# Kernel optimization log

Hardware: AMD Instinct MI355X
Metric: run time of the kernel (lower is better)

Reference implementation:

```python
import jax, jax.numpy as jnp
import numpy as np

STRIDES = (4, 8, 16, 32, 64)
FEAT = ((128, 128), (64, 64), (32, 32), (16, 16), (8, 8))
RATIOS = np.array([0.5, 1.0, 2.0], dtype=np.float64)
SCALE = 8.0
PRE_NMS = 2000
MAX_PER_IMG = 1000
NMS_THR = 0.7
MAX_SHAPE = (512, 512)
MAX_RATIO = float(abs(np.log(16.0 / 1000.0)))  # mmdet wh_ratio_clip default


def grid_anchors(H, W, stride):
    # mmdet AnchorGenerator: base_size = stride, center_offset = 0
    h_ratios = np.sqrt(RATIOS)
    w_ratios = 1.0 / h_ratios
    ws = stride * w_ratios * SCALE
    hs = stride * h_ratios * SCALE
    base = np.stack([-0.5 * ws, -0.5 * hs, 0.5 * ws, 0.5 * hs], axis=1)  # (A,4)
    sx = np.arange(W) * stride
    sy = np.arange(H) * stride
    yy, xx = np.meshgrid(sy, sx, indexing='ij')  # x varies fastest (mmdet order)
    shifts = np.stack([xx, yy, xx, yy], axis=-1).reshape(-1, 4)  # (H*W,4)
    return jnp.asarray((shifts[:, None, :] + base[None, :, :]).reshape(-1, 4), jnp.float32)


def level_candidates(cls, reg, anchors):
    # cls: (A,H,W), reg: (4A,H,W) -> location-major, anchor-minor flatten
    scores = jax.nn.sigmoid(jnp.transpose(cls, (1, 2, 0)).reshape(-1))
    deltas = jnp.transpose(reg, (1, 2, 0)).reshape(-1, 4)
    k = min(PRE_NMS, scores.shape[0])
    scores, idx = jax.lax.top_k(scores, k)
    return scores, deltas[idx], anchors[idx]


def decode(anchors, deltas):
    # DeltaXYWHBBoxCoder.decode with means=0, stds=1, max_shape=(512,512)
    px = (anchors[..., 0] + anchors[..., 2]) * 0.5
    py = (anchors[..., 1] + anchors[..., 3]) * 0.5
    pw = anchors[..., 2] - anchors[..., 0]
    ph = anchors[..., 3] - anchors[..., 1]
    dx, dy = deltas[..., 0], deltas[..., 1]
    dw = jnp.clip(deltas[..., 2], -MAX_RATIO, MAX_RATIO)
    dh = jnp.clip(deltas[..., 3], -MAX_RATIO, MAX_RATIO)
    gw = pw * jnp.exp(dw)
    gh = ph * jnp.exp(dh)
    gx = px + pw * dx
    gy = py + ph * dy
    x1 = jnp.clip(gx - gw * 0.5, 0.0, MAX_SHAPE[1])
    y1 = jnp.clip(gy - gh * 0.5, 0.0, MAX_SHAPE[0])
    x2 = jnp.clip(gx + gw * 0.5, 0.0, MAX_SHAPE[1])
    y2 = jnp.clip(gy + gh * 0.5, 0.0, MAX_SHAPE[0])
    return jnp.stack([x1, y1, x2, y2], axis=-1)


def nms_image(boxes, scores, levels):
    # boxes (M,4), scores (M,), levels (M,) int32. Fixed-shape greedy batched NMS;
    # invalid (zero-size, cf. filter_boxes with min_area=0) boxes get score -1 and are never kept.
    M = scores.shape[0]
    valid = ((boxes[:, 2] - boxes[:, 0]) > 0) & ((boxes[:, 3] - boxes[:, 1]) > 0)
    s = jnp.where(valid, scores, -1.0)
    order = jnp.argsort(-s)
    boxes_s = boxes[order]
    s = s[order]
    valid = valid[order]
    lev = levels[order]
    # batched_nms trick: offset each level so boxes of different levels never overlap
    off = lev.astype(boxes.dtype)[:, None] * (MAX_SHAPE[0] + 1.0)
    b = boxes_s + off
    x1, y1, x2, y2 = b[:, 0], b[:, 1], b[:, 2], b[:, 3]
    area = (x2 - x1) * (y2 - y1)
    iw = jnp.maximum(jnp.minimum(x2[:, None], x2[None, :]) - jnp.maximum(x1[:, None], x1[None, :]), 0.0)
    ih = jnp.maximum(jnp.minimum(y2[:, None], y2[None, :]) - jnp.maximum(y1[:, None], y1[None, :]), 0.0)
    inter = iw * ih
    union = area[:, None] + area[None, :] - inter
    iou = jnp.where(union > 0.0, inter / jnp.where(union > 0.0, union, 1.0), 0.0)  # (M,M)
    ar = jnp.arange(M)

    def body(i, keep):
        sup = keep[i] & (iou[i] > NMS_THR) & (ar > i)
        return keep & ~sup

    keep = jax.lax.fori_loop(0, M, body, valid)
    rank = jnp.cumsum(keep) - 1
    sel = keep & (rank < MAX_PER_IMG)
    dst = jnp.where(sel, rank, MAX_PER_IMG)  # overflow slot
    rows = jnp.concatenate([boxes_s, s[:, None]], axis=-1)
    rows = jnp.where(sel[:, None], rows, 0.0)
    out = jnp.zeros((MAX_PER_IMG + 1, 5), boxes.dtype).at[dst].set(rows)
    return out[:MAX_PER_IMG]


def setup_inputs() -> dict:
    key = jax.random.key(0)
    ks = jax.random.split(key, 10)
    d = {}
    for i, (h, w) in enumerate(FEAT):
        d[f'cls{i}'] = jax.random.normal(ks[i], (4, 3, h, w), dtype=jnp.float32)
        d[f'reg{i}'] = jax.random.normal(ks[5 + i], (4, 12, h, w), dtype=jnp.float32)
    return d


def reference(cls0, cls1, cls2, cls3, cls4, reg0, reg1, reg2, reg3, reg4):
    cls_list = [cls0, cls1, cls2, cls3, cls4]
    reg_list = [reg0, reg1, reg2, reg3, reg4]
    anchors = [grid_anchors(h, w, s) for (h, w), s in zip(FEAT, STRIDES)]
    sc, dl, an, lv = [], [], [], []
    for lvl in range(5):
        s, d, a = jax.vmap(level_candidates, in_axes=(0, 0, None))(cls_list[lvl], reg_list[lvl], anchors[lvl])
        sc.append(s); dl.append(d); an.append(a)
        lv.append(jnp.full(s.shape, lvl, jnp.int32))
    scores = jnp.concatenate(sc, axis=1)   # (N, M)
    deltas = jnp.concatenate(dl, axis=1)   # (N, M, 4)
    ancs = jnp.concatenate(an, axis=1)     # (N, M, 4)
    levels = jnp.concatenate(lv, axis=1)   # (N, M)
    boxes = decode(ancs, deltas)           # (N, M, 4)
    return jax.vmap(nms_image)(boxes, scores, levels)  # (N, 1000, 5)
```

## Files before the change

kernel.cpp:

```cpp
#include <hip/hip_runtime.h>
#include <cstdint>
#include <cstddef>

__constant__ int LV_N[5]    = {49152, 12288, 3072, 768, 192};
__constant__ int LV_K[5]    = {2000, 2000, 2000, 768, 192};
__constant__ int LV_OFF[5]  = {0, 2000, 4000, 6000, 6768};
__constant__ int LV_UOFF[5] = {0, 49152, 61440, 64512, 65280};
__constant__ int LV_W[5]    = {128, 64, 32, 16, 8};
__constant__ int LV_S[5]    = {4, 8, 16, 32, 64};
__constant__ int LV_LOGHW[5]= {14, 12, 10, 8, 6};
__constant__ int WPL[5]     = {32, 32, 32, 12, 3};
__constant__ int MOFF[5]    = {0, 70144, 140288, 210432, 221952};
__constant__ int MB_BASE[6] = {0, 256, 512, 768, 804, 807};
__constant__ int MB_CT[5]   = {8, 8, 8, 3, 1};
__constant__ int SGB6[6]    = {0, 12, 15, 16, 17, 18};

#define M_TOT 6960
#define U_PER_IMG 65472
#define MAX_OUT 1000
#define MWORDS_PER_IMG 223104
#define CAP 4096

struct Ptrs { const float* cls[5]; const float* reg[5]; };

#define MTH 0.7000000178813934326171875

__device__ __forceinline__ float xla_expf(float x) {
  const float exp_hi = 88.3762626647950f;
  const float exp_lo = -88.3762626647949f;
  const float log2ef = 1.44269504088896341f;
  const float c1 = 0.693359375f;
  const float c2 = -2.12194440e-4f;
  const float p0 = 1.9875691500e-4f;
  const float p1 = 1.3981999507e-3f;
  const float p2 = 8.3334519073e-3f;
  const float p3 = 4.1665795894e-2f;
  const float p4 = 1.6666665459e-1f;
  const float p5 = 5.0000001201e-1f;
  float xx = fminf(fmaxf(x, exp_lo), exp_hi);
  float fx = floorf(__fmaf_rn(xx, log2ef, 0.5f));
  float r = __fmaf_rn(fx, -c1, xx);
  r = __fmaf_rn(fx, -c2, r);
  float z = __fmul_rn(r, r);
  float y = __fmaf_rn(p0, r, p1);
  y = __fmaf_rn(y, r, p2);
  y = __fmaf_rn(y, r, p3);
  y = __fmaf_rn(y, r, p4);
  y = __fmaf_rn(y, r, p5);
  y = __fmaf_rn(y, z, r);
  y = __fadd_rn(y, 1.0f);
  int n = (int)fx;
  float two_n = __uint_as_float((unsigned)(n + 127) << 23);
  return __fmul_rn(y, two_n);
}

__device__ __forceinline__ float ref_sigmoid(float x) {
  return __fdiv_rn(1.0f, __fadd_rn(1.0f, xla_expf(-x)));
}

__global__ __launch_bounds__(256) void k_zero(uint4* ptr, int n4) {
  int i = (int)blockIdx.x * 256 + (int)threadIdx.x;
  if (i < n4) ptr[i] = make_uint4(0u, 0u, 0u, 0u);
}

__global__ __launch_bounds__(1024) void k_sig(Ptrs p, unsigned* u_arr,
                                              unsigned* ghist) {
  const int img = blockIdx.y;
  const int bx = blockIdx.x;
  int lvl = 0;
  while (bx >= SGB6[lvl + 1]) ++lvl;
  const int N = LV_N[lvl];
  const int e0 = (bx - SGB6[lvl]) * 4096;
  const int e1 = (e0 + 4096 < N) ? e0 + 4096 : N;
  const int tid = (int)threadIdx.x;
  __shared__ unsigned h[4096];
  for (int e = tid; e < 4096; e += 1024) h[e] = 0;
  __syncthreads();
  const float* cls = p.cls[lvl] + (size_t)img * N;
  unsigned* u = u_arr + img * U_PER_IMG + LV_UOFF[lvl];
  for (int e = e0 + tid; e < e1; e += 1024) {
    float logit = cls[e];
    unsigned ub = __float_as_uint(ref_sigmoid(logit));
    u[e] = ub;
    atomicAdd(&h[(ub >> 18) & 4095u], 1u);
  }
  __syncthreads();
  unsigned* gh = ghist + (size_t)(img * 5 + lvl) * 4096;
  for (int e = tid; e < 4096; e += 1024)
    if (h[e]) atomicAdd(&gh[e], h[e]);
}

__global__ __launch_bounds__(1024) void k_thresh(const unsigned* u_arr,
    const unsigned* ghist, unsigned long long* T64_arr) {
  const int blk = blockIdx.x;
  const int img = blk / 5, lvl = blk % 5;
  const int N = LV_N[lvl], K = LV_K[lvl], LOGHW = LV_LOGHW[lvl];
  const int HW = 1 << LOGHW;
  const int tid = (int)threadIdx.x;
  const int lane = tid & 63, w = tid >> 6;
  if (N <= K) { if (tid == 0) T64_arr[blk] = 0ULL; return; }
  __shared__ unsigned h[4096];
  __shared__ unsigned wsum[16], wsuf[16];
  __shared__ unsigned sh_D, sh_sD, sh_sD1;
  const unsigned* u = u_arr + img * U_PER_IMG + LV_UOFF[lvl];

  unsigned long long prefix = 0;
  unsigned want = (unsigned)K, above = 0;
  const int shifts[6] = {50, 38, 26, 14, 2, 0};
  for (int rd = 0; rd < 6; ++rd) {
    const int shift = shifts[rd];
    if (rd == 5) {
      for (int e = tid; e < 4; e += 1024) h[e] = 0;
      __syncthreads();
      for (int q = tid; q < N; q += 1024) {
        unsigned a = (unsigned)q >> LOGHW, pix = (unsigned)q & (unsigned)(HW - 1);
        unsigned ecl = pix * 3u + a;
        unsigned long long key =
            ((unsigned long long)u[q] << 32) | (unsigned)(~ecl);
        if ((key >> 2) == prefix) atomicAdd(&h[(unsigned)key & 3u], 1u);
      }
      __syncthreads();
      if (tid == 0) {
        unsigned cum = 0; int D = 0;
        for (int v = 3; v >= 0; --v) {
          if (cum + h[v] >= want) { D = v; break; }
          cum += h[v];
        }
        T64_arr[blk] = (prefix << 2) | (unsigned)D;
      }
      return;
    }
    if (rd == 0) {
      for (int e = tid; e < 4096; e += 1024)
        h[e] = ghist[(size_t)blk * 4096 + e];
    } else {
      for (int e = tid; e < 4096; e += 1024) h[e] = 0;
      __syncthreads();
      for (int q = tid; q < N; q += 1024) {
        unsigned a = (unsigned)q >> LOGHW, pix = (unsigned)q & (unsigned)(HW - 1);
        unsigned ecl = pix * 3u + a;
        unsigned long long key =
            ((unsigned long long)u[q] << 32) | (unsigned)(~ecl);
        if ((key >> (shift + 12)) == prefix)
          atomicAdd(&h[(unsigned)(key >> shift) & 4095u], 1u);
      }
    }
    __syncthreads();
    unsigned h0 = h[4 * tid + 0], h1 = h[4 * tid + 1];
    unsigned h2 = h[4 * tid + 2], h3 = h[4 * tid + 3];
    unsigned s = h0 + h1 + h2 + h3;
    unsigned suf = s;
    #pragma unroll
    for (int off = 1; off < 64; off <<= 1) {
      unsigned t2 = __shfl_down(suf, off);
      if (lane + off < 64) suf += t2;
    }
    if (lane == 0) wsum[w] = suf;
    __syncthreads();
    if (tid < 16) {
      unsigned v = wsum[tid];
      #pragma unroll
      for (int off = 1; off < 16; off <<= 1) {
        unsigned t2 = __shfl_down(v, off);
        if (tid + off < 16) v += t2;
      }
      wsuf[tid] = v;
    }
    __syncthreads();
    unsigned Sth = ((w + 1 < 16) ? wsuf[w + 1] : 0u) + (suf - s);
    unsigned f3 = Sth + h3;
    unsigned f2 = f3 + h2;
    unsigned f1 = f2 + h1;
    unsigned f0 = f1 + h0;
    if (f0 >= want && f1 < want) { sh_D = 4u * tid + 0; sh_sD = f0; sh_sD1 = f1; }
    if (f1 >= want && f2 < want) { sh_D = 4u * tid + 1; sh_sD = f1; sh_sD1 = f2; }
    if (f2 >= want && f3 < want) { sh_D = 4u * tid + 2; sh_sD = f2; sh_sD1 = f3; }
    if (f3 >= want && Sth < want) { sh_D = 4u * tid + 3; sh_sD = f3; sh_sD1 = Sth; }
    __syncthreads();
    unsigned D = sh_D, sD = sh_sD, sD1 = sh_sD1;
    unsigned long long npref = (prefix << 12) | (unsigned long long)D;
    if (above + sD <= (unsigned)CAP) {
      if (tid == 0) T64_arr[blk] = npref << shift;
      return;
    }
    above += sD1; want -= sD1; prefix = npref;
    __syncthreads();
  }
}

__global__ __launch_bounds__(1024) void k_collect(const unsigned* u_arr,
    const unsigned long long* T64_arr, unsigned long long* gtk, unsigned* gcnt) {
  const int img = blockIdx.y;
  const int bx = blockIdx.x;
  int lvl = 0;
  while (bx >= SGB6[lvl + 1]) ++lvl;
  const int N = LV_N[lvl], LOGHW = LV_LOGHW[lvl];
  const int HW = 1 << LOGHW;
  const int e0 = (bx - SGB6[lvl]) * 4096;
  const int tid = (int)threadIdx.x;
  const int lane = tid & 63;
  const int w = tid >> 6;
  const unsigned long long T = T64_arr[img * 5 + lvl];
  const unsigned* u = u_arr + img * U_PER_IMG + LV_UOFF[lvl];

  __shared__ unsigned wcnt[64];

  unsigned long long key0 = 0, key1 = 0, key2 = 0, key3 = 0;
  unsigned long long bm0, bm1, bm2, bm3;
  #define MKKEY(KV, Q)                                                      \
    {                                                                       \
      unsigned a_ = (unsigned)(Q) >> LOGHW;                                 \
      unsigned pix_ = (unsigned)(Q) & (unsigned)(HW - 1);                   \
      unsigned ecl_ = pix_ * 3u + a_;                                       \
      KV = ((unsigned long long)u[Q] << 32) | (unsigned)(~ecl_);            \
    }
  {
    int q = e0 + 0 * 1024 + tid;
    bool pr = false;
    if (q < N) { MKKEY(key0, q) pr = key0 >= T; }
    bm0 = __ballot(pr);
    if (lane == 0) wcnt[w * 4 + 0] = (unsigned)__popcll(bm0);
  }
  {
    int q = e0 + 1 * 1024 + tid;
    bool pr = false;
    if (q < N) { MKKEY(key1, q) pr = key1 >= T; }
    bm1 = __ballot(pr);
    if (lane == 0) wcnt[w * 4 + 1] = (unsigned)__popcll(bm1);
  }
  {
    int q = e0 + 2 * 1024 + tid;
    bool pr = false;
    if (q < N) { MKKEY(key2, q) pr = key2 >= T; }
    bm2 = __ballot(pr);
    if (lane == 0) wcnt[w * 4 + 2] = (unsigned)__popcll(bm2);
  }
  {
    int q = e0 + 3 * 1024 + tid;
    bool pr = false;
    if (q < N) { MKKEY(key3, q) pr = key3 >= T; }
    bm3 = __ballot(pr);
    if (lane == 0) wcnt[w * 4 + 3] = (unsigned)__popcll(bm3);
  }
  #undef MKKEY
  __syncthreads();
  if (tid < 64) {
    unsigned c = wcnt[tid];
    unsigned pre = c;
    #pragma unroll
    for (int off = 1; off < 64; off <<= 1) {
      unsigned t = __shfl_up(pre, off);
      if (tid >= off) pre += t;
    }
    unsigned total = __shfl(pre, 63);
    unsigned base = 0;
    if (tid == 63 && total) base = atomicAdd(gcnt + (img * 5 + lvl), total);
    base = __shfl(base, 63);
    wcnt[tid] = base + pre - c;
  }
  __syncthreads();
  unsigned long long* dst = gtk + (size_t)(img * 5 + lvl) * CAP;
  const unsigned long long below = (1ULL << lane) - 1ULL;
  if ((bm0 >> lane) & 1ULL) {
    unsigned slot = wcnt[w * 4 + 0] + (unsigned)__popcll(bm0 & below);
    if (slot < (unsigned)CAP) dst[slot] = key0;
  }
  if ((bm1 >> lane) & 1ULL) {
    unsigned slot = wcnt[w * 4 + 1] + (unsigned)__popcll(bm1 & below);
    if (slot < (unsigned)CAP) dst[slot] = key1;
  }
  if ((bm2 >> lane) & 1ULL) {
    unsigned slot = wcnt[w * 4 + 2] + (unsigned)__popcll(bm2 & below);
    if (slot < (unsigned)CAP) dst[slot] = key2;
  }
  if ((bm3 >> lane) & 1ULL) {
    unsigned slot = wcnt[w * 4 + 3] + (unsigned)__popcll(bm3 & below);
    if (slot < (unsigned)CAP) dst[slot] = key3;
  }
}

__global__ __launch_bounds__(256) void k_rank(Ptrs p,
    const unsigned long long* gtk, const unsigned* gcnt,
    float* cand_box, float* cand_s, unsigned long long* vflags) {
  const int il = (int)blockIdx.y;
  const int img = il / 5, lvl = il % 5;
  const int N = LV_N[lvl], K = LV_K[lvl], W = LV_W[lvl], S = LV_S[lvl];
  const int HW = N / 3;
  const float* reg = p.reg[lvl] + (size_t)img * 12 * HW;
  const int tid = (int)threadIdx.x;
  unsigned cnt = gcnt[il];
  if (cnt > (unsigned)CAP) cnt = CAP;
  if ((unsigned)blockIdx.x * 256u >= cnt) return;
  const unsigned cnt32 = (cnt + 31u) & ~31u;
  __shared__ ulonglong2 keys2[CAP / 2];
  unsigned long long* keys = (unsigned long long*)keys2;
  const unsigned long long* src = gtk + (size_t)il * CAP;
  for (int e = tid; e < (int)cnt32; e += 256)
    keys[e] = (e < (int)cnt) ? src[e] : 0ULL;
  __syncthreads();
  const int s = (int)blockIdx.x * 256 + tid;
  if (s >= (int)cnt) return;
  const unsigned long long mykey = keys[s];
  unsigned r0 = 0, r1 = 0, r2 = 0, r3 = 0;
  const unsigned half = cnt32 >> 1;
  for (unsigned j = 0; j < half; j += 16) {
    #pragma unroll
    for (int q = 0; q < 16; q += 4) {
      ulonglong2 a = keys2[j + q + 0];
      ulonglong2 b = keys2[j + q + 1];
      ulonglong2 cc = keys2[j + q + 2];
      ulonglong2 d = keys2[j + q + 3];
      r0 += (a.x > mykey ? 1u : 0u) + (a.y > mykey ? 1u : 0u);
      r1 += (b.x > mykey ? 1u : 0u) + (b.y > mykey ? 1u : 0u);
      r2 += (cc.x > mykey ? 1u : 0u) + (cc.y > mykey ? 1u : 0u);
      r3 += (d.x > mykey ? 1u : 0u) + (d.y > mykey ? 1u : 0u);
    }
  }
  unsigned rank = r0 + r1 + r2 + r3;
  if (rank >= (unsigned)K) return;

  unsigned ubits = (unsigned)(mykey >> 32);
  unsigned idx = ~((unsigned)mykey);
  int a = (int)(idx % 3u); int pix = (int)(idx / 3u);
  int xq = pix % W, yq = pix / W;
  float dx = reg[(a * 4 + 0) * HW + pix];
  float dy = reg[(a * 4 + 1) * HW + pix];
  float dw = reg[(a * 4 + 2) * HW + pix];
  float dh = reg[(a * 4 + 3) * HW + pix];
  double rr = (a == 0) ? 0.5 : (a == 1 ? 1.0 : 2.0);
  double hr = sqrt(rr), wr = 1.0 / hr;
  double st = (double)S;
  double wsd = st * wr * 8.0, hsd = st * hr * 8.0;
  double sxd = (double)(xq * S), syd = (double)(yq * S);
  float a0 = (float)(sxd - 0.5 * wsd), a1 = (float)(syd - 0.5 * hsd);
  float a2 = (float)(sxd + 0.5 * wsd), a3 = (float)(syd + 0.5 * hsd);
  float px = __fmul_rn(__fadd_rn(a0, a2), 0.5f);
  float py = __fmul_rn(__fadd_rn(a1, a3), 0.5f);
  float pw = __fsub_rn(a2, a0), ph = __fsub_rn(a3, a1);
  const float MRf = 4.135166556742356f;
  float dwc = fminf(fmaxf(dw, -MRf), MRf);
  float dhc = fminf(fmaxf(dh, -MRf), MRf);
  float gw = __fmul_rn(pw, xla_expf(dwc));
  float gh = __fmul_rn(ph, xla_expf(dhc));
  float gx = __fmaf_rn(pw, dx, px);
  float gy = __fmaf_rn(ph, dy, py);
  float x1 = fminf(fmaxf(__fmaf_rn(gw, -0.5f, gx), 0.0f), 512.0f);
  float y1 = fminf(fmaxf(__fmaf_rn(gh, -0.5f, gy), 0.0f), 512.0f);
  float x2 = fminf(fmaxf(__fmaf_rn(gw,  0.5f, gx), 0.0f), 512.0f);
  float y2 = fminf(fmaxf(__fmaf_rn(gh,  0.5f, gy), 0.0f), 512.0f);
  bool valid = (__fsub_rn(x2, x1) > 0.0f) && (__fsub_rn(y2, y1) > 0.0f);
  int pos = img * M_TOT + LV_OFF[lvl] + (int)rank;
  cand_box[(size_t)pos * 4 + 0] = x1;
  cand_box[(size_t)pos * 4 + 1] = y1;
  cand_box[(size_t)pos * 4 + 2] = x2;
  cand_box[(size_t)pos * 4 + 3] = y2;
  float score = __uint_as_float(ubits);
  cand_s[pos] = valid ? score : -1.0f;
  if (valid)
    atomicOr(&vflags[(size_t)il * 32 + (rank >> 6)], 1ULL << (rank & 63));
}

__global__ __launch_bounds__(256) void k_part(const float* cand_box,
    const float* cand_s, const unsigned long long* vflags,
    float* n_x1, float* n_y1, float* n_x2, float* n_y2, float* n_ar,
    float* n_sc, unsigned* n_pos, unsigned* V_arr) {
  const int il = (int)blockIdx.x;
  const int img = il / 5, lvl = il % 5;
  const int K = LV_K[lvl];
  const int tid = (int)threadIdx.x;
  __shared__ unsigned long long sflag[32];
  __shared__ unsigned wpre[33];
  if (tid < 32) sflag[tid] = vflags[(size_t)il * 32 + tid];
  __syncthreads();
  if (tid < 32) {
    unsigned c = (unsigned)__popcll(sflag[tid]);
    #pragma unroll
    for (int off = 1; off < 32; off <<= 1) {
      unsigned t = __shfl_up(c, off);
      if (tid >= off) c += t;
    }
    wpre[tid + 1] = c;
    if (tid == 0) wpre[0] = 0;
  }
  __syncthreads();
  const unsigned V = wpre[32];
  const float offv = __fmul_rn((float)lvl, 513.0f);
  const int base = img * M_TOT + LV_OFF[lvl];
  for (int r = tid; r < K; r += 256) {
    unsigned long long word = sflag[r >> 6];
    unsigned fl = (unsigned)((word >> (r & 63)) & 1ULL);
    unsigned excl = wpre[r >> 6] +
                    (unsigned)__popcll(word & ((1ULL << (r & 63)) - 1ULL));
    unsigned pdst = fl ? excl : V + ((unsigned)r - excl);
    const float* b = cand_box + (size_t)(base + r) * 4;
    float ox1 = __fadd_rn(b[0], offv), oy1 = __fadd_rn(b[1], offv);
    float ox2 = __fadd_rn(b[2], offv), oy2 = __fadd_rn(b[3], offv);
    int dst = base + (int)pdst;
    n_x1[dst] = ox1; n_y1[dst] = oy1; n_x2[dst] = ox2; n_y2[dst] = oy2;
    n_ar[dst] = __fmul_rn(__fsub_rn(ox2, ox1), __fsub_rn(oy2, oy1));
    n_sc[dst] = cand_s[base + r];
    n_pos[dst] = (unsigned)(LV_OFF[lvl] + r);
  }
  if (tid == 0) V_arr[il] = V;
}

#define TSTAGE(S, M)                                                        \
  {                                                                         \
    unsigned long long t_ = __shfl_xor(x, S);                               \
    x = (lane & S) ? ((x & (M)) | ((t_ >> S) & ~(M)))                       \
                   : ((x & ~(M)) | ((t_ << S) & (M)));                      \
  }

__global__ __launch_bounds__(256) void k_mask(
    const float* n_x1, const float* n_y1, const float* n_x2, const float* n_y2,
    const float* n_ar, unsigned long long* mask, unsigned long long* diagT) {
  const int img = blockIdx.y;
  const int bx = blockIdx.x;
  int lvl = 0;
  while (bx >= MB_BASE[lvl + 1]) ++lvl;
  const int t = bx - MB_BASE[lvl];
  const int ct = MB_CT[lvl];
  const int rt = t / ct, c = t % ct;
  const int K = LV_K[lvl];
  const int row0 = rt * 64, col0 = c * 256;
  if (col0 + 255 <= row0) return;

  __shared__ float4 cb4[256];
  __shared__ float cba[256];
  __shared__ float4 rb4[64];
  __shared__ float rba[64];
  const int base = img * M_TOT + LV_OFF[lvl];
  const int tid = (int)threadIdx.x;
  if (tid < 64) {
    int r = row0 + tid;
    if (r < K) {
      rb4[tid] = make_float4(n_x1[base + r], n_y1[base + r],
                             n_x2[base + r], n_y2[base + r]);
      rba[tid] = n_ar[base + r];
    } else {
      rb4[tid] = make_float4(0.f, 0.f, 0.f, 0.f);
      rba[tid] = 0.f;
    }
  }
  {
    int j = col0 + tid;
    if (j < K) {
      cb4[tid] = make_float4(n_x1[base + j], n_y1[base + j],
                             n_x2[base + j], n_y2[base + j]);
      cba[tid] = n_ar[base + j];
    }
  }
  __syncthreads();
  const int wl = tid >> 6, lane = tid & 63;
  const int r = row0 + lane;
  const bool rvalid = (r < K);
  const float4 rb = rb4[lane];
  const float rar = rba[lane];
  unsigned long long word = 0ULL;
  const int jbase = wl * 64;
  const int jmax = K - col0 - jbase;
  #pragma unroll 16
  for (int k = 0; k < 64; ++k) {
    float4 cb = cb4[jbase + k];
    float car = cba[jbase + k];
    float iw = fmaxf(__fsub_rn(fminf(rb.z, cb.z), fmaxf(rb.x, cb.x)), 0.0f);
    float ih = fmaxf(__fsub_rn(fminf(rb.w, cb.w), fmaxf(rb.y, cb.y)), 0.0f);
    float inter = __fmul_rn(iw, ih);
    float uni = __fsub_rn(__fadd_rn(rar, car), inter);
    bool sup = (uni > 0.0f) && ((double)inter >= MTH * (double)uni);
    if (sup && k < jmax) word |= (1ULL << k);
  }
  if (!rvalid) word = 0ULL;
  if (rvalid)
    mask[(size_t)img * MWORDS_PER_IMG + MOFF[lvl] +
         (size_t)r * WPL[lvl] + (size_t)((col0 >> 6) + wl)] = word;
  if (col0 + (wl << 6) == row0) {
    unsigned long long x = word;
    TSTAGE(32, 0xFFFFFFFF00000000ULL)
    TSTAGE(16, 0xFFFF0000FFFF0000ULL)
    TSTAGE(8,  0xFF00FF00FF00FF00ULL)
    TSTAGE(4,  0xF0F0F0F0F0F0F0F0ULL)
    TSTAGE(2,  0xCCCCCCCCCCCCCCCCULL)
    TSTAGE(1,  0xAAAAAAAAAAAAAAAAULL)
    diagT[(size_t)(img * 5 + lvl) * (40 * 64) + (size_t)rt * 64 + lane] = x;
  }
}

#define SCAN_CHUNK(P0, P1, P2, P3)                                          \
  {                                                                         \
    const int r0 = c << 6;                                                  \
    if (w == (c & 7)) {                                                     \
      unsigned long long v = (g == (c >> 3)) ? aw : ~0ULL;                  \
      v &= __shfl_xor(v, 1);                                                \
      v &= __shfl_xor(v, 2);                                                \
      v &= __shfl_xor(v, 4);                                                \
      v &= __shfl_xor(v, 8);                                                \
      v = __shfl(v, (c >> 3) * 16);                                         \
      unsigned long long x = dg;                                            \
      unsigned long long kw = v;                                            \
      while (true) {                                                        \
        bool keep_j = (((v >> lane) & 1ULL) != 0ULL) &&                     \
                      ((kw & below & x) == 0ULL);                           \
        unsigned long long nkw = __ballot(keep_j);                          \
        if (nkw == kw) break;                                               \
        kw = nkw;                                                           \
      }                                                                     \
      if ((kw >> lane) & 1ULL)                                              \
        skept[kept + (int)__popcll(kw & below)] = (unsigned)(r0 + lane);    \
      if (lane == 0) s_kw[c & 1] = kw;                                      \
      int no_ = next_own < 40 ? next_own : 39;                              \
      dg = dT[(size_t)no_ * 64 + lane];                                     \
      next_own += 8;                                                        \
    }                                                                       \
    __syncthreads();                                                        \
    unsigned long long kwv = s_kw[c & 1];                                   \
    kept += (int)__popcll(kwv);                                             \
    aw &= ~(P0 & (unsigned long long)((long long)(kwv << (63 - (d0 + 0))) >> 63)); \
    aw &= ~(P1 & (unsigned long long)((long long)(kwv << (63 - (d0 + 1))) >> 63)); \
    aw &= ~(P2 & (unsigned long long)((long long)(kwv << (63 - (d0 + 2))) >> 63)); \
    aw &= ~(P3 & (unsigned long long)((long long)(kwv << (63 - (d0 + 3))) >> 63)); \
    P0 = mb[(size_t)(r0 + 128 + d0 + 0) * wpl + wkc];                       \
    P1 = mb[(size_t)(r0 + 128 + d0 + 1) * wpl + wkc];                       \
    P2 = mb[(size_t)(r0 + 128 + d0 + 2) * wpl + wkc];                       \
    P3 = mb[(size_t)(r0 + 128 + d0 + 3) * wpl + wkc];                       \
    ++c;                                                                    \
  }

__global__ __launch_bounds__(512) void k_scan(const unsigned long long* mask,
    const unsigned long long* diagT,
    const unsigned* n_pos, const float* n_sc, const unsigned* V_arr,
    unsigned* kept_pos, unsigned long long* kept_key, unsigned* kept_cnt) {
  const int il = (int)blockIdx.x;
  const int img = il / 5, lvl = il % 5;
  const int K = LV_K[lvl], wpl = WPL[lvl];
  const int tid = (int)threadIdx.x;
  const int w = tid >> 6, lane = tid & 63;
  const unsigned long long* mb =
      mask + (size_t)img * MWORDS_PER_IMG + MOFF[lvl];
  const unsigned long long* dT = diagT + (size_t)il * (40 * 64);

  __shared__ unsigned long long s_kw[2];
  __shared__ unsigned skept[MAX_OUT + 64];

  const int g = lane >> 4;
  const int wk = w + 8 * g;
  const int wkc = wk < wpl ? wk : 0;
  const int d0 = (lane & 15) * 4;
  const unsigned long long below = (1ULL << lane) - 1ULL;

  const int V = (int)V_arr[il];
  unsigned long long aw;
  {
    int lo = wk * 64, hi = V < lo + 64 ? V : lo + 64;
    aw = (hi > lo) ? ((hi - lo == 64) ? ~0ULL : ((1ULL << (hi - lo)) - 1ULL))
                   : 0ULL;
  }

  const int nchunks = (K + 63) >> 6;
  unsigned long long pfA0 = mb[(size_t)(d0 + 0) * wpl + wkc];
  unsigned long long pfA1 = mb[(size_t)(d0 + 1) * wpl + wkc];
  unsigned long long pfA2 = mb[(size_t)(d0 + 2) * wpl + wkc];
  unsigned long long pfA3 = mb[(size_t)(d0 + 3) * wpl + wkc];
  unsigned long long pfB0 = mb[(size_t)(64 + d0 + 0) * wpl + wkc];
  unsigned long long pfB1 = mb[(size_t)(64 + d0 + 1) * wpl + wkc];
  unsigned long long pfB2 = mb[(size_t)(64 + d0 + 2) * wpl + wkc];
  unsigned long long pfB3 = mb[(size_t)(64 + d0 + 3) * wpl + wkc];
  unsigned long long dg = dT[(size_t)w * 64 + lane];
  int next_own = w + 8;

  int kept = 0;
  int c = 0;
  while (c < nchunks && kept < MAX_OUT) {
    SCAN_CHUNK(pfA0, pfA1, pfA2, pfA3)
    if (c >= nchunks || kept >= MAX_OUT) break;
    SCAN_CHUNK(pfB0, pfB1, pfB2, pfB3)
  }

  __syncthreads();
  const int kc = kept < MAX_OUT ? kept : MAX_OUT;
  const int base = img * M_TOT + LV_OFF[lvl];
  const size_t bo = (size_t)il * 1024;
  for (int i = tid; i < kc; i += 512) {
    unsigned r = skept[i];
    unsigned pp = n_pos[base + (int)r];
    kept_pos[bo + i] = pp;
    kept_key[bo + i] =
        ((unsigned long long)__float_as_uint(n_sc[base + (int)r]) << 32) |
        (unsigned)(~pp);
  }
  if (tid == 0) kept_cnt[il] = (unsigned)kc;
}

__global__ __launch_bounds__(1024) void k_merge(const float* cand_box,
    const float* cand_s, const unsigned* kept_pos,
    const unsigned long long* kept_key, const unsigned* kept_cnt, float* out) {
  const int il = (int)blockIdx.x;
  const int img = il / 5, l = il % 5;
  const int tid = (int)threadIdx.x;
  __shared__ unsigned cnts[5];
  __shared__ unsigned long long skey[5][1024];
  if (tid < 5) {
    unsigned c = kept_cnt[img * 5 + tid];
    cnts[tid] = c < (unsigned)MAX_OUT ? c : (unsigned)MAX_OUT;
  }
  __syncthreads();
  for (int e = tid; e < 5 * 1024; e += 1024) {
    int l2 = e >> 10, s = e & 1023;
    skey[l2][s] = (s < (int)cnts[l2])
        ? kept_key[(size_t)(img * 5 + l2) * 1024 + s] : 0ULL;
  }
  __syncthreads();
  if (l == 0) {
    unsigned T = cnts[0] + cnts[1] + cnts[2] + cnts[3] + cnts[4];
    unsigned Tc = T < (unsigned)MAX_OUT ? T : (unsigned)MAX_OUT;
    for (int r = (int)Tc + tid; r < MAX_OUT; r += 1024) {
      float* o = out + (size_t)img * (MAX_OUT * 5) + (size_t)r * 5;
      o[0] = 0.f; o[1] = 0.f; o[2] = 0.f; o[3] = 0.f; o[4] = 0.f;
    }
  }
  const int s = tid;
  if (s >= (int)cnts[l]) return;
  unsigned long long k0 = skey[l][s];
  unsigned rank = (unsigned)s;
  #pragma unroll
  for (int l2 = 0; l2 < 5; ++l2) {
    if (l2 == l) continue;
    int lo = 0, hi = (int)cnts[l2];
    while (lo < hi) {
      int mid = (lo + hi) >> 1;
      if (skey[l2][mid] > k0) lo = mid + 1; else hi = mid;
    }
    rank += (unsigned)lo;
  }
  if (rank < (unsigned)MAX_OUT) {
    unsigned pos = kept_pos[(size_t)(img * 5 + l) * 1024 + s];
    const float* b = cand_box + (size_t)(img * M_TOT + pos) * 4;
    float* o = out + (size_t)img * (MAX_OUT * 5) + (size_t)rank * 5;
    o[0] = b[0]; o[1] = b[1]; o[2] = b[2]; o[3] = b[3];
    o[4] = cand_s[img * M_TOT + pos];
  }
}

extern "C" void kernel_launch(void* const* d_in, const int* in_sizes, int n_in,
                              void* d_out, int out_size, void* d_ws, size_t ws_size,
                              hipStream_t stream) {
  Ptrs p;
  bool interleaved = (n_in == 10 && in_sizes[1] == 4 * 12 * 128 * 128);
  for (int l = 0; l < 5; ++l) {
    if (interleaved) {
      p.cls[l] = (const float*)d_in[2 * l];
      p.reg[l] = (const float*)d_in[2 * l + 1];
    } else {
      p.cls[l] = (const float*)d_in[l];
      p.reg[l] = (const float*)d_in[5 + l];
    }
  }
  uint8_t* w = (uint8_t*)d_ws;
  size_t o = 0;
  auto carve = [&](size_t bytes) {
    void* ptr = w + o;
    o += (bytes + 255) & ~(size_t)255;
    return ptr;
  };
  unsigned* gcnt = (unsigned*)carve((size_t)20 * 4);
  unsigned* ghist = (unsigned*)carve((size_t)20 * 4096 * 4);
  unsigned long long* vflags = (unsigned long long*)carve((size_t)20 * 32 * 8);
  size_t zero_bytes = 256 + (size_t)20 * 4096 * 4 + (size_t)20 * 32 * 8;
  unsigned long long* T64_arr = (unsigned long long*)carve((size_t)20 * 8);
  unsigned* u_arr = (unsigned*)carve((size_t)4 * U_PER_IMG * 4);
  float* cand_box = (float*)carve((size_t)4 * M_TOT * 4 * 4);
  float* cand_s = (float*)carve((size_t)4 * M_TOT * 4);
  float* n_x1 = (float*)carve((size_t)4 * M_TOT * 4);
  float* n_y1 = (float*)carve((size_t)4 * M_TOT * 4);
  float* n_x2 = (float*)carve((size_t)4 * M_TOT * 4);
  float* n_y2 = (float*)carve((size_t)4 * M_TOT * 4);
  float* n_ar = (float*)carve((size_t)4 * M_TOT * 4);
  float* n_sc = (float*)carve((size_t)4 * M_TOT * 4);
  unsigned* n_pos = (unsigned*)carve((size_t)4 * M_TOT * 4);
  unsigned* V_arr = (unsigned*)carve((size_t)20 * 4);
  unsigned* kept_pos = (unsigned*)carve((size_t)4 * 5 * 1024 * 4);
  unsigned long long* kept_key = (unsigned long long*)carve((size_t)4 * 5 * 1024 * 8);
  unsigned* kept_cnt = (unsigned*)carve((size_t)20 * 4);
  unsigned long long* diagT = (unsigned long long*)carve((size_t)20 * 40 * 64 * 8);
  unsigned long long* mask = (unsigned long long*)carve((size_t)4 * MWORDS_PER_IMG * 8);
  unsigned long long* gtk = mask;
  (void)ws_size; (void)out_size;

  int n4 = (int)(zero_bytes >> 4);
  k_zero<<<(n4 + 255) / 256, 256, 0, stream>>>((uint4*)gcnt, n4);
  k_sig<<<dim3(18, 4), 1024, 0, stream>>>(p, u_arr, ghist);
  k_thresh<<<20, 1024, 0, stream>>>(u_arr, ghist, T64_arr);
  k_collect<<<dim3(18, 4), 1024, 0, stream>>>(u_arr, T64_arr, gtk, gcnt);
  k_rank<<<dim3(16, 20), 256, 0, stream>>>(p, gtk, gcnt, cand_box, cand_s,
                                           vflags);
  k_part<<<20, 256, 0, stream>>>(cand_box, cand_s, vflags,
      n_x1, n_y1, n_x2, n_y2, n_ar, n_sc, n_pos, V_arr);
  k_mask<<<dim3(807, 4), 256, 0, stream>>>(n_x1, n_y1, n_x2, n_y2, n_ar,
                                           mask, diagT);
  k_scan<<<20, 512, 0, stream>>>(mask, diagT, n_pos, n_sc, V_arr,
                                 kept_pos, kept_key, kept_cnt);
  k_merge<<<20, 1024, 0, stream>>>(cand_box, cand_s, kept_pos, kept_key,
                                   kept_cnt, (float*)d_out);
}
```

Measured before the change: 116.5 us.

## Drop zeroing kernel via per-block histograms and skip lower-triangle mask waves

The separate zero-fill kernel is removed. Each sigmoid block now writes its own private 4096-bin histogram with plain stores, and the threshold kernel sums those histograms into registers, so the global histogram no longer needs zeroing or global atomics. The vflags and gcnt counters are zeroed inside the sigmoid kernel instead. In the NMS mask kernel, waves whose column range lies entirely at or below the row block return early, skipping IoU work the scan presumably never reads. This saves a launch and some atomic traffic, at the cost of a larger histogram buffer and a correctness dependence on those mask words going unused.

```diff
diff --git a/kernel.cpp b/kernel.cpp
--- a/kernel.cpp
+++ b/kernel.cpp
@@ -58,13 +58,8 @@
   return __fdiv_rn(1.0f, __fadd_rn(1.0f, xla_expf(-x)));
 }
 
-__global__ __launch_bounds__(256) void k_zero(uint4* ptr, int n4) {
-  int i = (int)blockIdx.x * 256 + (int)threadIdx.x;
-  if (i < n4) ptr[i] = make_uint4(0u, 0u, 0u, 0u);
-}
-
 __global__ __launch_bounds__(1024) void k_sig(Ptrs p, unsigned* u_arr,
-                                              unsigned* ghist) {
+    unsigned* ghist, unsigned long long* vflags, unsigned* gcnt) {
   const int img = blockIdx.y;
   const int bx = blockIdx.x;
   int lvl = 0;
@@ -73,6 +68,10 @@
   const int e0 = (bx - SGB6[lvl]) * 4096;
   const int e1 = (e0 + 4096 < N) ? e0 + 4096 : N;
   const int tid = (int)threadIdx.x;
+  if (bx == 0) {
+    if (tid < 160) vflags[(size_t)img * 160 + tid] = 0ULL;
+    if (tid < 5) gcnt[img * 5 + tid] = 0u;
+  }
   __shared__ unsigned h[4096];
   for (int e = tid; e < 4096; e += 1024) h[e] = 0;
   __syncthreads();
@@ -85,9 +84,8 @@
     atomicAdd(&h[(ub >> 18) & 4095u], 1u);
   }
   __syncthreads();
-  unsigned* gh = ghist + (size_t)(img * 5 + lvl) * 4096;
-  for (int e = tid; e < 4096; e += 1024)
-    if (h[e]) atomicAdd(&gh[e], h[e]);
+  unsigned* gh = ghist + ((size_t)(img * 18 + bx) << 12);
+  for (int e = tid; e < 4096; e += 1024) gh[e] = h[e];
 }
 
 __global__ __launch_bounds__(1024) void k_thresh(const unsigned* u_arr,
@@ -130,9 +128,14 @@
       }
       return;
     }
+    unsigned h0, h1, h2, h3;
     if (rd == 0) {
-      for (int e = tid; e < 4096; e += 1024)
-        h[e] = ghist[(size_t)blk * 4096 + e];
+      h0 = h1 = h2 = h3 = 0;
+      for (int t = SGB6[lvl]; t < SGB6[lvl + 1]; ++t) {
+        const uint4* g4 = (const uint4*)(ghist + ((size_t)(img * 18 + t) << 12));
+        uint4 v = g4[tid];
+        h0 += v.x; h1 += v.y; h2 += v.z; h3 += v.w;
+      }
     } else {
       for (int e = tid; e < 4096; e += 1024) h[e] = 0;
       __syncthreads();
@@ -144,10 +147,10 @@
         if ((key >> (shift + 12)) == prefix)
           atomicAdd(&h[(unsigned)(key >> shift) & 4095u], 1u);
       }
-    }
-    __syncthreads();
-    unsigned h0 = h[4 * tid + 0], h1 = h[4 * tid + 1];
-    unsigned h2 = h[4 * tid + 2], h3 = h[4 * tid + 3];
+      __syncthreads();
+      h0 = h[4 * tid + 0]; h1 = h[4 * tid + 1];
+      h2 = h[4 * tid + 2]; h3 = h[4 * tid + 3];
+    }
     unsigned s = h0 + h1 + h2 + h3;
     unsigned suf = s;
     #pragma unroll
@@ -452,6 +455,7 @@
   }
   __syncthreads();
   const int wl = tid >> 6, lane = tid & 63;
+  if (col0 + (wl << 6) + 63 <= row0) return;
   const int r = row0 + lane;
   const bool rvalid = (r < K);
   const float4 rb = rb4[lane];
@@ -663,9 +667,8 @@
     return ptr;
   };
   unsigned* gcnt = (unsigned*)carve((size_t)20 * 4);
-  unsigned* ghist = (unsigned*)carve((size_t)20 * 4096 * 4);
+  unsigned* ghist = (unsigned*)carve((size_t)72 * 4096 * 4);
   unsigned long long* vflags = (unsigned long long*)carve((size_t)20 * 32 * 8);
-  size_t zero_bytes = 256 + (size_t)20 * 4096 * 4 + (size_t)20 * 32 * 8;
   unsigned long long* T64_arr = (unsigned long long*)carve((size_t)20 * 8);
   unsigned* u_arr = (unsigned*)carve((size_t)4 * U_PER_IMG * 4);
   float* cand_box = (float*)carve((size_t)4 * M_TOT * 4 * 4);
@@ -686,9 +689,7 @@
   unsigned long long* gtk = mask;
   (void)ws_size; (void)out_size;
 
-  int n4 = (int)(zero_bytes >> 4);
-  k_zero<<<(n4 + 255) / 256, 256, 0, stream>>>((uint4*)gcnt, n4);
-  k_sig<<<dim3(18, 4), 1024, 0, stream>>>(p, u_arr, ghist);
+  k_sig<<<dim3(18, 4), 1024, 0, stream>>>(p, u_arr, ghist, vflags, gcnt);
   k_thresh<<<20, 1024, 0, stream>>>(u_arr, ghist, T64_arr);
   k_collect<<<dim3(18, 4), 1024, 0, stream>>>(u_arr, T64_arr, gtk, gcnt);
   k_rank<<<dim3(16, 20), 256, 0, stream>>>(p, gtk, gcnt, cand_box, cand_s,
```

Result: no change. 114.3 us (-1.9%).
